# Kernel tuning notes

Hardware: AMD Instinct MI355X
Metric: run time of the kernel (lower is better)

The kernel has to match this reference:

```python
import jax, jax.numpy as jnp
import numpy as np

N = 50000
E = 800000
IN_DIM = 128
HID = 32
HEADS = 4
NEG_SLOPE = 0.2


def setup_inputs() -> dict:
    key = jax.random.key(0)
    ks = jax.random.split(key, 12)
    x = jax.random.normal(ks[0], (N, IN_DIM), dtype=jnp.float32)
    edge_index = jax.random.randint(ks[1], (2, E), 0, N, dtype=jnp.int64)
    s1 = 1.0 / np.sqrt(IN_DIM)
    s2 = 1.0 / np.sqrt(HEADS * HID)
    W1 = jax.random.normal(ks[2], (IN_DIM, HEADS * HID), dtype=jnp.float32) * s1
    a_src1 = jax.random.normal(ks[3], (HEADS, HID), dtype=jnp.float32) * s1
    a_dst1 = jax.random.normal(ks[4], (HEADS, HID), dtype=jnp.float32) * s1
    b1 = jnp.zeros((HEADS * HID,), dtype=jnp.float32)
    W2 = jax.random.normal(ks[5], (HEADS * HID, HID), dtype=jnp.float32) * s2
    a_src2 = jax.random.normal(ks[6], (1, HID), dtype=jnp.float32) * s2
    a_dst2 = jax.random.normal(ks[7], (1, HID), dtype=jnp.float32) * s2
    b2 = jnp.zeros((HID,), dtype=jnp.float32)
    return {"x": x, "edge_index": edge_index, "W1": W1, "a_src1": a_src1,
            "a_dst1": a_dst1, "b1": b1, "W2": W2, "a_src2": a_src2,
            "a_dst2": a_dst2, "b2": b2}


def _gat_layer(x, W, a_src, a_dst, bias, src, dst, heads, ch):
    n = x.shape[0]
    h = (x @ W).reshape(n, heads, ch)                    # [N,H,C]
    # per-node attention halves (GATv1): a_src . h_i, a_dst . h_j
    al_s = jnp.einsum('nhc,hc->nh', h, a_src)            # [N,H]
    al_d = jnp.einsum('nhc,hc->nh', h, a_dst)
    e = jax.nn.leaky_relu(al_s[src] + al_d[dst], NEG_SLOPE)  # [E,H]
    # segment softmax over edges sharing the same destination
    e_max = jax.ops.segment_max(e, dst, num_segments=n)
    e_exp = jnp.exp(e - e_max[dst])
    denom = jax.ops.segment_sum(e_exp, dst, num_segments=n)
    alpha = e_exp / (denom[dst] + 1e-16)                 # [E,H]
    msg = h[src] * alpha[:, :, None]                     # [E,H,C]
    out = jax.ops.segment_sum(msg, dst, num_segments=n)  # [N,H,C]
    return out.reshape(n, heads * ch) + bias


def reference(x, edge_index, W1, a_src1, a_dst1, b1, W2, a_src2, a_dst2, b2):
    n = x.shape[0]
    # PyG GATConv adds self-loops by default
    loops = jnp.arange(n, dtype=edge_index.dtype)
    src = jnp.concatenate([edge_index[0], loops])
    dst = jnp.concatenate([edge_index[1], loops])
    h = _gat_layer(x, W1, a_src1, a_dst1, b1, src, dst, HEADS, HID)
    h = jax.nn.elu(h)
    out = _gat_layer(h, W2, a_src2, a_dst2, b2, src, dst, 1, HID)
    return out
```

## Files before the change

kernel.cpp:

```cpp
#include <hip/hip_runtime.h>
#include <hip/hip_bf16.h>

#define NN 50000
#define EE 800000
#define EN (EE + NN)
#define IN_DIM 128
#define HID 32
#define HEADS 4
#define F1 (HEADS * HID)
#define NEG 0.2f
#define SLOT 64

typedef __hip_bfloat16 bf16;
typedef __bf16 bf16x8 __attribute__((ext_vector_type(8)));
typedef float f32x4 __attribute__((ext_vector_type(4)));

__device__ __forceinline__ float cvt(float v) { return v; }
__device__ __forceinline__ float cvt(bf16 v)  { return __bfloat162float(v); }

__device__ __forceinline__ float bflo(unsigned u) {
    union { unsigned u; float f; } v; v.u = u << 16; return v.f;
}
__device__ __forceinline__ float bfhi(unsigned u) {
    union { unsigned u; float f; } v; v.u = u & 0xFFFF0000u; return v.f;
}

__device__ __forceinline__ unsigned short f2bf_bits(float f) {
    union { float f; unsigned u; } v; v.f = f;
    unsigned r = v.u + 0x7FFFu + ((v.u >> 16) & 1u);
    return (unsigned short)(r >> 16);
}

__device__ __forceinline__ unsigned short f2h_bits(float f) {
    _Float16 h = (_Float16)f;
    union { _Float16 h; unsigned short s; } v; v.h = h; return v.s;
}
__device__ __forceinline__ float h2f(unsigned short s) {
    union { _Float16 h; unsigned short s; } v; v.s = s; return (float)v.h;
}

#define ZERO_B ((NN + 255) / 256)
#define PREP_B (1 + ZERO_B + 16 + 1)

__global__ void k_prep(const void* xv, const void* eiv,
                       const void* W1v, const void* W2v,
                       int* __restrict__ flags, int* __restrict__ counts,
                       unsigned short* __restrict__ W1T,
                       unsigned short* __restrict__ W2T) {
    const int b = blockIdx.x, t = threadIdx.x;
    if (b == 0) {
        if (t < 64) {
            const unsigned* xw = (const unsigned*)xv;
            const unsigned* ew = (const unsigned*)eiv;
            int lo_nz = 0, huge = 0, hi_nz = 0;
            for (int j = 0; j < 4; ++j) {
                unsigned w = xw[t * 4 + j];
                unsigned lo = w & 0xFFFFu;
                if (lo != 0u) lo_nz = 1;
                if (((lo >> 7) & 0xFFu) >= 0xC0u) huge = 1;
                unsigned eo = ew[(t * 4 + j) * 2 + 1];
                if (eo != 0u) hi_nz = 1;
            }
            unsigned long long m_lo = __ballot(lo_nz);
            unsigned long long m_hg = __ballot(huge);
            unsigned long long m_hi = __ballot(hi_nz);
            if (t == 0) {
                flags[0] = (m_lo == 0ull || m_hg != 0ull) ? 1 : 0;
                flags[1] = (m_hi == 0ull) ? 1 : 0;
            }
        }
        return;
    }
    if (b <= ZERO_B) {
        int i = (b - 1) * 256 + t;
        if (i < NN) counts[i] = 0;
        return;
    }
    __shared__ int sf;
    if (t < 64) {
        const unsigned* xw = (const unsigned*)xv;
        int lo_nz = 0, huge = 0;
        for (int j = 0; j < 4; ++j) {
            unsigned w = xw[t * 4 + j];
            unsigned lo = w & 0xFFFFu;
            if (lo != 0u) lo_nz = 1;
            if (((lo >> 7) & 0xFFu) >= 0xC0u) huge = 1;
        }
        unsigned long long m_lo = __ballot(lo_nz);
        unsigned long long m_hg = __ballot(huge);
        if (t == 0) sf = (m_lo == 0ull || m_hg != 0ull) ? 1 : 0;
    }
    __syncthreads();
    const int f32in = sf;
    const int tb = b - 1 - ZERO_B;
    if (tb < 16) {
        const unsigned short* wg = (const unsigned short*)W1v;
        const float* wf = (const float*)W1v;
        for (int i = 0; i < 4; ++i) {
            int j = tb * 1024 + i * 256 + t;
            int k = j >> 7, n = j & 127;
            W1T[n * 128 + k] = f32in ? f2bf_bits(wf[j]) : wg[j];
        }
    } else {
        const unsigned short* wg = (const unsigned short*)W2v;
        const float* wf = (const float*)W2v;
        for (int i = 0; i < 16; ++i) {
            int j = i * 256 + t;
            int k = j >> 5, n = j & 31;
            W2T[n * 128 + k] = f32in ? f2bf_bits(wf[j]) : wg[j];
        }
    }
}

#define QUAD_B ((EN / 4 + 255) / 256)

__global__ void k_hist(const void* ei, const int* __restrict__ flags,
                       int* __restrict__ counts, int* __restrict__ srcs2) {
    int p = blockIdx.x * 256 + threadIdx.x;
    int i4 = p * 4;
    if (i4 >= EN) return;
    int s0, s1, s2, s3, d0, d1, d2, d3;
    if (i4 >= EE) {
        s0 = d0 = i4 - EE; s1 = d1 = s0 + 1; s2 = d2 = s0 + 2; s3 = d3 = s0 + 3;
    } else if (flags[1]) {
        const long long* e64 = (const long long*)ei;
        long2 sa = *(const long2*)&e64[i4];
        long2 sb = *(const long2*)&e64[i4 + 2];
        long2 da = *(const long2*)&e64[EE + i4];
        long2 db = *(const long2*)&e64[EE + i4 + 2];
        s0 = (int)sa.x; s1 = (int)sa.y; s2 = (int)sb.x; s3 = (int)sb.y;
        d0 = (int)da.x; d1 = (int)da.y; d2 = (int)db.x; d3 = (int)db.y;
    } else {
        const int* e32 = (const int*)ei;
        int4 ss = *(const int4*)&e32[i4];
        int4 dd = *(const int4*)&e32[EE + i4];
        s0 = ss.x; s1 = ss.y; s2 = ss.z; s3 = ss.w;
        d0 = dd.x; d1 = dd.y; d2 = dd.z; d3 = dd.w;
    }
    int r0 = atomicAdd(&counts[d0], 1);
    int r1 = atomicAdd(&counts[d1], 1);
    int r2 = atomicAdd(&counts[d2], 1);
    int r3 = atomicAdd(&counts[d3], 1);
    if (r0 < SLOT) srcs2[d0 * SLOT + r0] = s0;
    if (r1 < SLOT) srcs2[d1 * SLOT + r1] = s1;
    if (r2 < SLOT) srcs2[d2 * SLOT + r2] = s2;
    if (r3 < SLOT) srcs2[d3 * SLOT + r3] = s3;
}

#define MROWS 64
#define LDK 136

__global__ __launch_bounds__(256) void k_lin1_mfma(
    const void* xv, const unsigned short* __restrict__ W1T,
    const void* as1v, const void* ad1v,
    const int* __restrict__ flags, unsigned* __restrict__ h1,
    float* __restrict__ als, float* __restrict__ ald)
{
    __shared__ __align__(16) char smem[(MROWS + 128) * LDK * 2];
    unsigned short* xs  = (unsigned short*)smem;
    unsigned short* w1t = xs + MROWS * LDK;
    float* hs = (float*)smem;
    __shared__ float sa[F1], sd[F1];

    const int t = threadIdx.x;
    const int row0 = blockIdx.x * MROWS;
    const int f32in = flags[0];

    if (t < F1) {
        sa[t] = f32in ? ((const float*)as1v)[t] : cvt(((const bf16*)as1v)[t]);
        sd[t] = f32in ? ((const float*)ad1v)[t] : cvt(((const bf16*)ad1v)[t]);
    }
    if (!f32in) {
        const uint4* xg = (const uint4*)xv;
        for (int i = 0; i < 4; ++i) {
            int id = i * 256 + t;
            int m = id >> 4, seg = id & 15;
            int gr = row0 + m;
            uint4 val = (gr < NN) ? xg[(size_t)gr * 16 + seg] : make_uint4(0, 0, 0, 0);
            *(uint4*)&xs[m * LDK + seg * 8] = val;
        }
    } else {
        const float4* xf = (const float4*)xv;
        for (int i = 0; i < 8; ++i) {
            int id = i * 256 + t;
            int m = id >> 5, c = id & 31;
            int gr = row0 + m;
            float4 v = (gr < NN) ? xf[(size_t)gr * 32 + c]
                                 : make_float4(0.f, 0.f, 0.f, 0.f);
            unsigned w0 = (unsigned)f2bf_bits(v.x) | ((unsigned)f2bf_bits(v.y) << 16);
            unsigned w1 = (unsigned)f2bf_bits(v.z) | ((unsigned)f2bf_bits(v.w) << 16);
            *(uint2*)&xs[m * LDK + c * 4] = make_uint2(w0, w1);
        }
    }
    {
        const uint4* wg = (const uint4*)W1T;
        for (int i = 0; i < 8; ++i) {
            int id = i * 256 + t;
            int n = id >> 4, seg = id & 15;
            *(uint4*)&w1t[n * LDK + seg * 8] = wg[id];
        }
    }
    __syncthreads();

    const int wave = t >> 6, lane = t & 63, quad = lane >> 4, l16 = lane & 15;
    f32x4 acc[8];
#pragma unroll
    for (int ni = 0; ni < 8; ++ni) acc[ni] = (f32x4){0.f, 0.f, 0.f, 0.f};

    const int arow = wave * 16 + l16;
#pragma unroll
    for (int kc = 0; kc < 4; ++kc) {
        int ko = kc * 32 + quad * 8;
        bf16x8 av = *(const bf16x8*)&xs[arow * LDK + ko];
#pragma unroll
        for (int ni = 0; ni < 8; ++ni) {
            bf16x8 bv = *(const bf16x8*)&w1t[(ni * 16 + l16) * LDK + ko];
            acc[ni] = __builtin_amdgcn_mfma_f32_16x16x32_bf16(av, bv, acc[ni], 0, 0, 0);
        }
    }
    __syncthreads();

#pragma unroll
    for (int ni = 0; ni < 8; ++ni)
#pragma unroll
        for (int r = 0; r < 4; ++r) {
            int m = wave * 16 + quad * 4 + r;
            hs[m * 132 + ni * 16 + l16] = acc[ni][r];
        }
    __syncthreads();

    for (int i = 0; i < 16; ++i) {
        int id = i * 256 + t;
        int m = id >> 6, wd = id & 63;
        int gr = row0 + m;
        if (gr < NN) {
            unsigned pw = (unsigned)f2bf_bits(hs[m * 132 + 2 * wd]) |
                          ((unsigned)f2bf_bits(hs[m * 132 + 2 * wd + 1]) << 16);
            h1[(size_t)gr * 64 + wd] = pw;
        }
    }
    {
        int m = t >> 2, h = t & 3;
        int gr = row0 + m;
        if (gr < NN) {
            float ps = 0.f, pd = 0.f;
#pragma unroll
            for (int j = 0; j < 32; ++j) {
                float v = hs[m * 132 + h * 32 + j];
                ps += v * sa[h * 32 + j];
                pd += v * sd[h * 32 + j];
            }
            als[gr * 4 + h] = ps;
            ald[gr * 4 + h] = pd;
        }
    }
}

__global__ __launch_bounds__(256) void k_agg1(
    const int* __restrict__ counts, const int* __restrict__ srcs2,
    const float* __restrict__ als, const float* __restrict__ ald,
    const bf16* __restrict__ h1, const void* b1v, const int* __restrict__ flags,
    uint4* __restrict__ hm)
{
    const int lane = threadIdx.x & 63;
    const int d = blockIdx.x * 4 + (threadIdx.x >> 6);
    const int q = lane >> 4;
    const int u = lane & 15;
    const int h = u >> 2;
    const int start = d * SLOT;
    const int end = start + min(counts[d], SLOT);
    const uint4* rows = (const uint4*)h1;
    const float advh = ald[d * 4 + h];

    float A[8] = {0,0,0,0,0,0,0,0}, B[8] = {0,0,0,0,0,0,0,0};
    float DA = 0.f, DB = 0.f;
    int e = start + q;
    for (; e + 4 < end; e += 8) {
        int s0 = srcs2[e], s1 = srcs2[e + 4];
        float e0 = als[s0 * 4 + h] + advh;
        float e1 = als[s1 * 4 + h] + advh;
        e0 = e0 > 0.f ? e0 : NEG * e0;
        e1 = e1 > 0.f ? e1 : NEG * e1;
        float x0 = __expf(e0), x1 = __expf(e1);
        uint4 u0 = rows[(size_t)s0 * 16 + u];
        uint4 u1 = rows[(size_t)s1 * 16 + u];
        A[0] += x0 * bflo(u0.x); A[1] += x0 * bfhi(u0.x);
        A[2] += x0 * bflo(u0.y); A[3] += x0 * bfhi(u0.y);
        A[4] += x0 * bflo(u0.z); A[5] += x0 * bfhi(u0.z);
        A[6] += x0 * bflo(u0.w); A[7] += x0 * bfhi(u0.w); DA += x0;
        B[0] += x1 * bflo(u1.x); B[1] += x1 * bfhi(u1.x);
        B[2] += x1 * bflo(u1.y); B[3] += x1 * bfhi(u1.y);
        B[4] += x1 * bflo(u1.z); B[5] += x1 * bfhi(u1.z);
        B[6] += x1 * bflo(u1.w); B[7] += x1 * bfhi(u1.w); DB += x1;
    }
    for (; e < end; e += 4) {
        int s0 = srcs2[e];
        float e0 = als[s0 * 4 + h] + advh;
        e0 = e0 > 0.f ? e0 : NEG * e0;
        float x0 = __expf(e0);
        uint4 u0 = rows[(size_t)s0 * 16 + u];
        A[0] += x0 * bflo(u0.x); A[1] += x0 * bfhi(u0.x);
        A[2] += x0 * bflo(u0.y); A[3] += x0 * bfhi(u0.y);
        A[4] += x0 * bflo(u0.z); A[5] += x0 * bfhi(u0.z);
        A[6] += x0 * bflo(u0.w); A[7] += x0 * bfhi(u0.w); DA += x0;
    }
    float a[8];
#pragma unroll
    for (int j = 0; j < 8; ++j) a[j] = A[j] + B[j];
    float dsum = DA + DB;
#pragma unroll
    for (int j = 0; j < 8; ++j) {
        a[j] += __shfl_xor(a[j], 16);
        a[j] += __shfl_xor(a[j], 32);
    }
    dsum += __shfl_xor(dsum, 16);
    dsum += __shfl_xor(dsum, 32);
    if (q == 0) {
        float inv = 1.f / (dsum + 1e-16f);
        float bb[8];
        if (flags[0]) {
            float4 b0 = ((const float4*)b1v)[2 * u];
            float4 b1 = ((const float4*)b1v)[2 * u + 1];
            bb[0] = b0.x; bb[1] = b0.y; bb[2] = b0.z; bb[3] = b0.w;
            bb[4] = b1.x; bb[5] = b1.y; bb[6] = b1.z; bb[7] = b1.w;
        } else {
            uint4 ub = ((const uint4*)b1v)[u];
            bb[0] = bflo(ub.x); bb[1] = bfhi(ub.x); bb[2] = bflo(ub.y); bb[3] = bfhi(ub.y);
            bb[4] = bflo(ub.z); bb[5] = bfhi(ub.z); bb[6] = bflo(ub.w); bb[7] = bfhi(ub.w);
        }
        float v[8];
#pragma unroll
        for (int j = 0; j < 8; ++j) {
            float vv = a[j] * inv + bb[j];
            v[j] = vv > 0.f ? vv : (__expf(vv) - 1.f);
        }
        uint4 w;
        w.x = (unsigned)f2bf_bits(v[0]) | ((unsigned)f2bf_bits(v[1]) << 16);
        w.y = (unsigned)f2bf_bits(v[2]) | ((unsigned)f2bf_bits(v[3]) << 16);
        w.z = (unsigned)f2bf_bits(v[4]) | ((unsigned)f2bf_bits(v[5]) << 16);
        w.w = (unsigned)f2bf_bits(v[6]) | ((unsigned)f2bf_bits(v[7]) << 16);
        hm[(size_t)d * 16 + u] = w;
    }
}

__global__ __launch_bounds__(256) void k_mid_mfma(
    const bf16* __restrict__ hm, const unsigned short* __restrict__ W2T,
    const void* as2v, const void* ad2v,
    const int* __restrict__ flags, unsigned short* __restrict__ h2,
    float* __restrict__ als2, float* __restrict__ ald2)
{
    __shared__ __align__(16) unsigned short hs[MROWS * LDK];
    __shared__ __align__(16) unsigned short w2t[32 * LDK];
    __shared__ float sa2[HID], sd2[HID];

    const int t = threadIdx.x;
    const int row0 = blockIdx.x * MROWS;
    const int f32in = flags[0];

    if (t < HID) {
        sa2[t] = f32in ? ((const float*)as2v)[t] : cvt(((const bf16*)as2v)[t]);
        sd2[t] = f32in ? ((const float*)ad2v)[t] : cvt(((const bf16*)ad2v)[t]);
    }
    {
        const uint4* hg = (const uint4*)hm;
        for (int i = 0; i < 4; ++i) {
            int id = i * 256 + t;
            int m = id >> 4, seg = id & 15;
            int gr = row0 + m;
            uint4 val = (gr < NN) ? hg[(size_t)gr * 16 + seg] : make_uint4(0, 0, 0, 0);
            *(uint4*)&hs[m * LDK + seg * 8] = val;
        }
        const uint4* wg = (const uint4*)W2T;
        for (int i = 0; i < 2; ++i) {
            int id = i * 256 + t;
            int n = id >> 4, seg = id & 15;
            *(uint4*)&w2t[n * LDK + seg * 8] = wg[id];
        }
    }
    __syncthreads();

    const int wave = t >> 6, lane = t & 63, quad = lane >> 4, l16 = lane & 15;
    f32x4 acc[2];
    acc[0] = (f32x4){0.f, 0.f, 0.f, 0.f};
    acc[1] = (f32x4){0.f, 0.f, 0.f, 0.f};
    const int arow = wave * 16 + l16;
#pragma unroll
    for (int kc = 0; kc < 4; ++kc) {
        int ko = kc * 32 + quad * 8;
        bf16x8 av = *(const bf16x8*)&hs[arow * LDK + ko];
#pragma unroll
        for (int ni = 0; ni < 2; ++ni) {
            bf16x8 bv = *(const bf16x8*)&w2t[(ni * 16 + l16) * LDK + ko];
            acc[ni] = __builtin_amdgcn_mfma_f32_16x16x32_bf16(av, bv, acc[ni], 0, 0, 0);
        }
    }

#pragma unroll
    for (int ni = 0; ni < 2; ++ni)
#pragma unroll
        for (int r = 0; r < 4; ++r) {
            int gr = row0 + wave * 16 + quad * 4 + r;
            if (gr < NN) h2[(size_t)gr * 32 + ni * 16 + l16] = f2h_bits(acc[ni][r]);
        }

    float ps[4], pd[4];
#pragma unroll
    for (int r = 0; r < 4; ++r) {
        ps[r] = acc[0][r] * sa2[l16] + acc[1][r] * sa2[16 + l16];
        pd[r] = acc[0][r] * sd2[l16] + acc[1][r] * sd2[16 + l16];
    }
#pragma unroll
    for (int mask = 1; mask < 16; mask <<= 1)
#pragma unroll
        for (int r = 0; r < 4; ++r) {
            ps[r] += __shfl_xor(ps[r], mask);
            pd[r] += __shfl_xor(pd[r], mask);
        }
    if (l16 == 0) {
#pragma unroll
        for (int r = 0; r < 4; ++r) {
            int gr = row0 + wave * 16 + quad * 4 + r;
            if (gr < NN) { als2[gr] = ps[r]; ald2[gr] = pd[r]; }
        }
    }
}

__global__ __launch_bounds__(256) void k_agg2(
    const int* __restrict__ counts, const int* __restrict__ srcs2,
    const float* __restrict__ als2, const float* __restrict__ ald2,
    const uint2* __restrict__ h2,
    const void* b2v, const int* __restrict__ flags, void* out)
{
    const int lane = threadIdx.x & 63;
    const int node = blockIdx.x * 4 + (threadIdx.x >> 6);
    const int q = lane >> 3;
    const int u = lane & 7;
    const int start = node * SLOT;
    const int end = start + min(counts[node], SLOT);
    const float adv = ald2[node];

    float A0 = 0.f, A1 = 0.f, A2 = 0.f, A3 = 0.f, D0 = 0.f;
    for (int e = start + q; e < end; e += 8) {
        int s0 = srcs2[e];
        float e0 = als2[s0] + adv;
        e0 = e0 > 0.f ? e0 : NEG * e0;
        float x0 = __expf(e0);
        uint2 w = h2[(size_t)s0 * 8 + u];
        A0 += x0 * h2f((unsigned short)(w.x & 0xFFFFu));
        A1 += x0 * h2f((unsigned short)(w.x >> 16));
        A2 += x0 * h2f((unsigned short)(w.y & 0xFFFFu));
        A3 += x0 * h2f((unsigned short)(w.y >> 16));
        D0 += x0;
    }
    A0 += __shfl_xor(A0, 8);  A1 += __shfl_xor(A1, 8);
    A2 += __shfl_xor(A2, 8);  A3 += __shfl_xor(A3, 8);  D0 += __shfl_xor(D0, 8);
    A0 += __shfl_xor(A0, 16); A1 += __shfl_xor(A1, 16);
    A2 += __shfl_xor(A2, 16); A3 += __shfl_xor(A3, 16); D0 += __shfl_xor(D0, 16);
    A0 += __shfl_xor(A0, 32); A1 += __shfl_xor(A1, 32);
    A2 += __shfl_xor(A2, 32); A3 += __shfl_xor(A3, 32); D0 += __shfl_xor(D0, 32);
    if (q == 0) {
        float inv = 1.f / (D0 + 1e-16f);
        float r0 = A0 * inv, r1 = A1 * inv, r2 = A2 * inv, r3 = A3 * inv;
        if (flags[0]) {
            float4 bb = ((const float4*)b2v)[u];
            ((float4*)out)[(size_t)node * 8 + u] =
                make_float4(r0 + bb.x, r1 + bb.y, r2 + bb.z, r3 + bb.w);
        } else {
            uint2 ub = ((const uint2*)b2v)[u];
            r0 += bflo(ub.x); r1 += bfhi(ub.x); r2 += bflo(ub.y); r3 += bfhi(ub.y);
            unsigned w0 = (unsigned)f2bf_bits(r0) | ((unsigned)f2bf_bits(r1) << 16);
            unsigned w1 = (unsigned)f2bf_bits(r2) | ((unsigned)f2bf_bits(r3) << 16);
            ((uint2*)out)[(size_t)node * 8 + u] = make_uint2(w0, w1);
        }
    }
}

extern "C" void kernel_launch(void* const* d_in, const int* in_sizes, int n_in,
                              void* d_out, int out_size, void* d_ws, size_t ws_size,
                              hipStream_t stream) {
    const void* x    = d_in[0];
    const void* ei   = d_in[1];
    const void* W1   = d_in[2];
    const void* a_s1 = d_in[3];
    const void* a_d1 = d_in[4];
    const void* b1   = d_in[5];
    const void* W2   = d_in[6];
    const void* a_s2 = d_in[7];
    const void* a_d2 = d_in[8];
    const void* b2v  = d_in[9];

    int*   flags  = (int*)d_ws;
    char*  pc     = (char*)d_ws + 256;
    uint4* hm     = (uint4*)pc;            pc += (size_t)NN * 16 * 16;
    bf16*  h1     = (bf16*)pc;             pc += (size_t)NN * F1 * 2;
    unsigned short* h2 = (unsigned short*)h1;
    int*   srcs2  = (int*)pc;              pc += (size_t)NN * SLOT * 4;
    float* al_s1  = (float*)pc;            pc += (size_t)NN * HEADS * 4;
    float* al_d1  = (float*)pc;            pc += (size_t)NN * HEADS * 4;
    float* al_s2  = (float*)pc;            pc += (size_t)NN * 4;
    float* al_d2  = (float*)pc;            pc += (size_t)NN * 4;
    int*   counts = (int*)pc;              pc += (size_t)NN * 4;
    unsigned short* W1T = (unsigned short*)pc; pc += (size_t)128 * 128 * 2;
    unsigned short* W2T = (unsigned short*)pc; pc += (size_t)32 * 128 * 2;

    k_prep<<<PREP_B, 256, 0, stream>>>(x, ei, W1, W2, flags, counts, W1T, W2T);
    k_hist<<<QUAD_B, 256, 0, stream>>>(ei, flags, counts, srcs2);
    k_lin1_mfma<<<(NN + MROWS - 1) / MROWS, 256, 0, stream>>>(x, W1T, a_s1, a_d1,
                                                              flags, (unsigned*)h1,
                                                              al_s1, al_d1);
    k_agg1<<<NN / 4, 256, 0, stream>>>(counts, srcs2, al_s1, al_d1, h1, b1,
                                       flags, hm);
    k_mid_mfma<<<(NN + MROWS - 1) / MROWS, 256, 0, stream>>>((const bf16*)hm, W2T, a_s2,
                                                             a_d2, flags, h2, al_s2, al_d2);
    k_agg2<<<NN / 4, 256, 0, stream>>>(counts, srcs2, al_s2, al_d2,
                                       (const uint2*)h2, b2v, flags, d_out);
}
```

Baseline: 230.8 us.

## Fuse edge histogram into lin1 MFMA kernel via block-range split

```diff
diff --git a/kernel.cpp b/kernel.cpp
--- a/kernel.cpp
+++ b/kernel.cpp
@@ -112,50 +112,37 @@
     }
 }
 
-#define QUAD_B ((EN / 4 + 255) / 256)
-
-__global__ void k_hist(const void* ei, const int* __restrict__ flags,
-                       int* __restrict__ counts, int* __restrict__ srcs2) {
-    int p = blockIdx.x * 256 + threadIdx.x;
-    int i4 = p * 4;
-    if (i4 >= EN) return;
-    int s0, s1, s2, s3, d0, d1, d2, d3;
-    if (i4 >= EE) {
-        s0 = d0 = i4 - EE; s1 = d1 = s0 + 1; s2 = d2 = s0 + 2; s3 = d3 = s0 + 3;
-    } else if (flags[1]) {
-        const long long* e64 = (const long long*)ei;
-        long2 sa = *(const long2*)&e64[i4];
-        long2 sb = *(const long2*)&e64[i4 + 2];
-        long2 da = *(const long2*)&e64[EE + i4];
-        long2 db = *(const long2*)&e64[EE + i4 + 2];
-        s0 = (int)sa.x; s1 = (int)sa.y; s2 = (int)sb.x; s3 = (int)sb.y;
-        d0 = (int)da.x; d1 = (int)da.y; d2 = (int)db.x; d3 = (int)db.y;
-    } else {
-        const int* e32 = (const int*)ei;
-        int4 ss = *(const int4*)&e32[i4];
-        int4 dd = *(const int4*)&e32[EE + i4];
-        s0 = ss.x; s1 = ss.y; s2 = ss.z; s3 = ss.w;
-        d0 = dd.x; d1 = dd.y; d2 = dd.z; d3 = dd.w;
-    }
-    int r0 = atomicAdd(&counts[d0], 1);
-    int r1 = atomicAdd(&counts[d1], 1);
-    int r2 = atomicAdd(&counts[d2], 1);
-    int r3 = atomicAdd(&counts[d3], 1);
-    if (r0 < SLOT) srcs2[d0 * SLOT + r0] = s0;
-    if (r1 < SLOT) srcs2[d1 * SLOT + r1] = s1;
-    if (r2 < SLOT) srcs2[d2 * SLOT + r2] = s2;
-    if (r3 < SLOT) srcs2[d3 * SLOT + r3] = s3;
-}
-
 #define MROWS 64
 #define LDK 136
-
-__global__ __launch_bounds__(256) void k_lin1_mfma(
-    const void* xv, const unsigned short* __restrict__ W1T,
+#define LIN_B ((NN + MROWS - 1) / MROWS)
+#define EDGE_B ((EN + 255) / 256)
+#define FUSE_B (LIN_B + EDGE_B)
+
+__global__ __launch_bounds__(256) void k_fused(
+    const void* xv, const void* eiv, const unsigned short* __restrict__ W1T,
     const void* as1v, const void* ad1v,
-    const int* __restrict__ flags, unsigned* __restrict__ h1,
+    const int* __restrict__ flags,
+    int* __restrict__ counts, int* __restrict__ srcs2,
+    unsigned* __restrict__ h1,
     float* __restrict__ als, float* __restrict__ ald)
 {
+    if (blockIdx.x >= LIN_B) {
+        int idx = (blockIdx.x - LIN_B) * 256 + threadIdx.x;
+        if (idx >= EN) return;
+        int s, d;
+        if (idx >= EE) { s = d = idx - EE; }
+        else if (flags[1]) {
+            const long long* e64 = (const long long*)eiv;
+            s = (int)e64[idx]; d = (int)e64[EE + idx];
+        } else {
+            const int* e32 = (const int*)eiv;
+            s = e32[idx]; d = e32[EE + idx];
+        }
+        int r = atomicAdd(&counts[d], 1);
+        if (r < SLOT) srcs2[d * SLOT + r] = s;
+        return;
+    }
+
     __shared__ __align__(16) char smem[(MROWS + 128) * LDK * 2];
     unsigned short* xs  = (unsigned short*)smem;
     unsigned short* w1t = xs + MROWS * LDK;
@@ -504,10 +491,8 @@
     unsigned short* W2T = (unsigned short*)pc; pc += (size_t)32 * 128 * 2;
 
     k_prep<<<PREP_B, 256, 0, stream>>>(x, ei, W1, W2, flags, counts, W1T, W2T);
-    k_hist<<<QUAD_B, 256, 0, stream>>>(ei, flags, counts, srcs2);
-    k_lin1_mfma<<<(NN + MROWS - 1) / MROWS, 256, 0, stream>>>(x, W1T, a_s1, a_d1,
-                                                              flags, (unsigned*)h1,
-                                                              al_s1, al_d1);
+    k_fused<<<FUSE_B, 256, 0, stream>>>(x, ei, W1T, a_s1, a_d1, flags,
+                                        counts, srcs2, (unsigned*)h1, al_s1, al_d1);
     k_agg1<<<NN / 4, 256, 0, stream>>>(counts, srcs2, al_s1, al_d1, h1, b1,
                                        flags, hm);
     k_mid_mfma<<<(NN + MROWS - 1) / MROWS, 256, 0, stream>>>((const bf16*)hm, W2T, a_s2,
```

Result: no change. 233.2 us (+1.0%).

## Split edge histogram into atomic rank pass and separate scatter pass

Applied to the files above, without the earlier changes.

```diff
diff --git a/kernel.cpp b/kernel.cpp
--- a/kernel.cpp
+++ b/kernel.cpp
@@ -112,39 +112,50 @@
     }
 }
 
-#define QUAD_B ((EN / 4 + 255) / 256)
+#define PAIR_B ((EN / 2 + 255) / 256)
 
 __global__ void k_hist(const void* ei, const int* __restrict__ flags,
-                       int* __restrict__ counts, int* __restrict__ srcs2) {
+                       int* __restrict__ counts, int* __restrict__ rank) {
     int p = blockIdx.x * 256 + threadIdx.x;
-    int i4 = p * 4;
-    if (i4 >= EN) return;
-    int s0, s1, s2, s3, d0, d1, d2, d3;
-    if (i4 >= EE) {
-        s0 = d0 = i4 - EE; s1 = d1 = s0 + 1; s2 = d2 = s0 + 2; s3 = d3 = s0 + 3;
-    } else if (flags[1]) {
+    int i2 = p * 2;
+    if (i2 >= EN) return;
+    int d0, d1;
+    if (i2 >= EE) { d0 = i2 - EE; d1 = d0 + 1; }
+    else if (flags[1]) {
         const long long* e64 = (const long long*)ei;
-        long2 sa = *(const long2*)&e64[i4];
-        long2 sb = *(const long2*)&e64[i4 + 2];
-        long2 da = *(const long2*)&e64[EE + i4];
-        long2 db = *(const long2*)&e64[EE + i4 + 2];
-        s0 = (int)sa.x; s1 = (int)sa.y; s2 = (int)sb.x; s3 = (int)sb.y;
-        d0 = (int)da.x; d1 = (int)da.y; d2 = (int)db.x; d3 = (int)db.y;
+        long2 dd = *(const long2*)&e64[EE + i2];
+        d0 = (int)dd.x; d1 = (int)dd.y;
     } else {
         const int* e32 = (const int*)ei;
-        int4 ss = *(const int4*)&e32[i4];
-        int4 dd = *(const int4*)&e32[EE + i4];
-        s0 = ss.x; s1 = ss.y; s2 = ss.z; s3 = ss.w;
-        d0 = dd.x; d1 = dd.y; d2 = dd.z; d3 = dd.w;
+        int2 dd = *(const int2*)&e32[EE + i2];
+        d0 = dd.x; d1 = dd.y;
     }
     int r0 = atomicAdd(&counts[d0], 1);
     int r1 = atomicAdd(&counts[d1], 1);
-    int r2 = atomicAdd(&counts[d2], 1);
-    int r3 = atomicAdd(&counts[d3], 1);
-    if (r0 < SLOT) srcs2[d0 * SLOT + r0] = s0;
-    if (r1 < SLOT) srcs2[d1 * SLOT + r1] = s1;
-    if (r2 < SLOT) srcs2[d2 * SLOT + r2] = s2;
-    if (r3 < SLOT) srcs2[d3 * SLOT + r3] = s3;
+    *(int2*)&rank[i2] = make_int2(r0, r1);
+}
+
+__global__ void k_scatter(const void* ei, const int* __restrict__ flags,
+                          const int* __restrict__ rank, int* __restrict__ srcs2) {
+    int p = blockIdx.x * 256 + threadIdx.x;
+    int i2 = p * 2;
+    if (i2 >= EN) return;
+    int s0, s1, d0, d1;
+    if (i2 >= EE) { s0 = d0 = i2 - EE; s1 = d1 = s0 + 1; }
+    else if (flags[1]) {
+        const long long* e64 = (const long long*)ei;
+        long2 ss = *(const long2*)&e64[i2];
+        long2 dd = *(const long2*)&e64[EE + i2];
+        s0 = (int)ss.x; s1 = (int)ss.y; d0 = (int)dd.x; d1 = (int)dd.y;
+    } else {
+        const int* e32 = (const int*)ei;
+        int2 ss = *(const int2*)&e32[i2];
+        int2 dd = *(const int2*)&e32[EE + i2];
+        s0 = ss.x; s1 = ss.y; d0 = dd.x; d1 = dd.y;
+    }
+    int2 rr = *(const int2*)&rank[i2];
+    if (rr.x < SLOT) srcs2[d0 * SLOT + rr.x] = s0;
+    if (rr.y < SLOT) srcs2[d1 * SLOT + rr.y] = s1;
 }
 
 #define MROWS 64
@@ -245,7 +256,8 @@
         if (gr < NN) {
             float ps = 0.f, pd = 0.f;
 #pragma unroll
-            for (int j = 0; j < 32; ++j) {
+            for (int jj = 0; jj < 32; ++jj) {
+                int j = (jj + 8 * h) & 31;
                 float v = hs[m * 132 + h * 32 + j];
                 ps += v * sa[h * 32 + j];
                 pd += v * sd[h * 32 + j];
@@ -492,6 +504,7 @@
     int*   flags  = (int*)d_ws;
     char*  pc     = (char*)d_ws + 256;
     uint4* hm     = (uint4*)pc;            pc += (size_t)NN * 16 * 16;
+    int*   rank   = (int*)hm;
     bf16*  h1     = (bf16*)pc;             pc += (size_t)NN * F1 * 2;
     unsigned short* h2 = (unsigned short*)h1;
     int*   srcs2  = (int*)pc;              pc += (size_t)NN * SLOT * 4;
@@ -504,7 +517,8 @@
     unsigned short* W2T = (unsigned short*)pc; pc += (size_t)32 * 128 * 2;
 
     k_prep<<<PREP_B, 256, 0, stream>>>(x, ei, W1, W2, flags, counts, W1T, W2T);
-    k_hist<<<QUAD_B, 256, 0, stream>>>(ei, flags, counts, srcs2);
+    k_hist<<<PAIR_B, 256, 0, stream>>>(ei, flags, counts, rank);
+    k_scatter<<<PAIR_B, 256, 0, stream>>>(ei, flags, rank, srcs2);
     k_lin1_mfma<<<(NN + MROWS - 1) / MROWS, 256, 0, stream>>>(x, W1T, a_s1, a_d1,
                                                               flags, (unsigned*)h1,
                                                               al_s1, al_d1);
```

After: 220.6 us. -4.4%, faster.
